# Optimization experiments

Hardware: AMD Instinct MI355X
Metric: run time of the kernel (lower is better)

## Reference

```python
import jax, jax.numpy as jnp
import numpy as np

B, S, D, H, MRP = 2, 2048, 1024, 16, 128
DK = D // H
NUM_REL = 2 * MRP + 1


def setup_inputs() -> dict:
    key = jax.random.key(0)
    ks = jax.random.split(key, 14)
    w = lambda k, shp: (jax.random.normal(k, shp, jnp.float32) * 0.02)
    return {
        'query': jax.random.normal(ks[0], (B, S, D), jnp.float32),
        'key':   jax.random.normal(ks[1], (B, S, D), jnp.float32),
        'value': jax.random.normal(ks[2], (B, S, D), jnp.float32),
        'Wq': w(ks[3], (D, D)), 'bq': jnp.zeros((D,), jnp.float32),
        'Wk': w(ks[4], (D, D)), 'bk': jnp.zeros((D,), jnp.float32),
        'Wv': w(ks[5], (D, D)), 'bv': jnp.zeros((D,), jnp.float32),
        'Wo': w(ks[6], (D, D)), 'bo': jnp.zeros((D,), jnp.float32),
        'rel_k': w(ks[7], (NUM_REL, DK)),
        'rel_v': w(ks[8], (NUM_REL, DK)),
    }


def reference(query, key, value, Wq, bq, Wk, bk, Wv, bv, Wo, bo, rel_k, rel_v):
    b, s, d = query.shape
    h, dk = H, DK
    # projections -> (b, h, s, dk)
    Q = (query @ Wq.T + bq).reshape(b, s, h, dk).transpose(0, 2, 1, 3)
    K = (key   @ Wk.T + bk).reshape(b, s, h, dk).transpose(0, 2, 1, 3)
    V = (value @ Wv.T + bv).reshape(b, s, h, dk).transpose(0, 2, 1, 3)
    # relative position indices: distance(i,j) = j - i, clipped, shifted to [0, 2*MRP]
    pos = jnp.arange(s)
    rel_idx = jnp.clip(pos[None, :] - pos[:, None], -MRP, MRP) + MRP  # (s, s)
    rk = rel_k[rel_idx]  # (s, s, dk)
    rv = rel_v[rel_idx]  # (s, s, dk)
    # content scores + relative-key scores
    scores = jnp.einsum('bhqd,bhkd->bhqk', Q, K)
    scores = scores + jnp.einsum('bhqd,qkd->bhqk', Q, rk)
    scores = scores * (1.0 / np.sqrt(dk).astype(np.float32))
    attn = jax.nn.softmax(scores, axis=-1)  # (b, h, s, s)
    # content context + relative-value context
    ctx = jnp.einsum('bhqk,bhkd->bhqd', attn, V)
    ctx = ctx + jnp.einsum('bhqk,qkd->bhqd', attn, rv)
    ctx = ctx.transpose(0, 2, 1, 3).reshape(b, s, d)
    out = ctx @ Wo.T + bo
    return out, attn
```

## Files before the change

kernel.cpp:

```cpp
#include <hip/hip_runtime.h>
#include <hip/hip_bf16.h>
#include <cstdint>
#include <cstddef>

using u16 = unsigned short;
using u32 = unsigned int;

typedef float f32x4 __attribute__((ext_vector_type(4)));
typedef short s16x8 __attribute__((ext_vector_type(8)));
typedef _Float16 f16x8 __attribute__((ext_vector_type(8)));
typedef unsigned short u16x4 __attribute__((ext_vector_type(4)));
typedef u32 u32x4 __attribute__((ext_vector_type(4)));

constexpr int Bc  = 2;
constexpr int Sc  = 2048;
constexpr int Dc  = 1024;
constexpr int Hc  = 16;
constexpr int DKc = 64;
constexpr int BHc = Bc * Hc;
constexpr int NREL = 257;
constexpr int RKROWS = 272;
constexpr int RVCOLS = 288;

constexpr float QSCALE = 0.125f * 1.4426950408889634f;

__device__ __forceinline__ u16 f2bf(float x){
  return __builtin_bit_cast(u16, __float2bfloat16(x));
}
__device__ __forceinline__ float bf2f(u16 u){
  return __builtin_bit_cast(float, (u32)u << 16);
}
__device__ __forceinline__ u16 f2h(float x){
  return __builtin_bit_cast(u16, (_Float16)x);
}
__device__ __forceinline__ u32 packh2(float a, float b){
  u16 x = __builtin_bit_cast(u16, (_Float16)a);
  u16 y = __builtin_bit_cast(u16, (_Float16)b);
  return (u32)x | ((u32)y << 16);
}
__device__ __forceinline__ float h2f_lo(u32 w){
  return (float)__builtin_bit_cast(_Float16, (u16)(w & 0xffffu));
}
__device__ __forceinline__ float h2f_hi(u32 w){
  return (float)__builtin_bit_cast(_Float16, (u16)(w >> 16));
}
__device__ __forceinline__ f32x4 mfma16(s16x8 a, s16x8 b, f32x4 c){
  return __builtin_amdgcn_mfma_f32_16x16x32_bf16(a, b, c, 0, 0, 0);
}
__device__ __forceinline__ f32x4 mfma16h(f16x8 a, f16x8 b, f32x4 c){
  return __builtin_amdgcn_mfma_f32_16x16x32_f16(a, b, c, 0, 0, 0);
}
__device__ __forceinline__ s16x8 ld8(const u16* p){
  return *reinterpret_cast<const s16x8*>(p);
}
__device__ __forceinline__ f16x8 ld8h(const u16* p){
  return *reinterpret_cast<const f16x8*>(p);
}
__device__ __forceinline__ void st_bf8(u16* p, float4 a, float4 b){
  s16x8 t;
  t[0] = (short)f2bf(a.x); t[1] = (short)f2bf(a.y);
  t[2] = (short)f2bf(a.z); t[3] = (short)f2bf(a.w);
  t[4] = (short)f2bf(b.x); t[5] = (short)f2bf(b.y);
  t[6] = (short)f2bf(b.z); t[7] = (short)f2bf(b.w);
  *reinterpret_cast<s16x8*>(p) = t;
}

__global__ void prep_rel(const float* __restrict__ rel_k,
                         const float* __restrict__ rel_v,
                         u16* __restrict__ relkb, u16* __restrict__ relvT)
{
  int tid = blockIdx.x * blockDim.x + threadIdx.x;
  int nthr = gridDim.x * blockDim.x;
  for (int i = tid; i < RKROWS * DKc; i += nthr){
    int r = i >> 6, c = i & 63;
    float v = (r < NREL) ? rel_k[r * DKc + c] : 0.0f;
    relkb[i] = f2bf(v);
  }
  for (int i = tid; i < DKc * RVCOLS; i += nthr){
    int d = i / RVCOLS, j = i - d * RVCOLS;
    float v = (j < NREL) ? rel_v[j * DKc + d] : 0.0f;
    relvT[i] = f2h(v);
  }
}

__global__ __launch_bounds__(256, 4) void proj_gemm(
    const float* __restrict__ Xq, const float* __restrict__ Xk, const float* __restrict__ Xv,
    const float* __restrict__ Wq, const float* __restrict__ Wk, const float* __restrict__ Wv,
    const float* __restrict__ bq, const float* __restrict__ bk, const float* __restrict__ bv,
    u16* __restrict__ Qb, u16* __restrict__ Kb, u16* __restrict__ Vt)
{
  const int type = blockIdx.y;
  const float* X    = (type == 0) ? Xq : (type == 1) ? Xk : Xv;
  const float* W    = (type == 0) ? Wq : (type == 1) ? Wk : Wv;
  const float* bias = (type == 0) ? bq : (type == 1) ? bk : bv;

  const int m0 = (int)(blockIdx.x >> 4) * 64;
  const int n0 = (int)(blockIdx.x & 15) * 64;

  __shared__ alignas(16) u16 As[64][56];
  __shared__ alignas(16) u16 Bs[64][56];

  const int tid  = threadIdx.x;
  const int wid  = tid >> 6, lane = tid & 63;
  const int lgrp = lane >> 4, lidx = lane & 15;
  const int wr   = wid >> 1,  wc   = wid & 1;

  const int srow = tid >> 2;
  const int scol = (tid & 3) << 3;

  f32x4 acc[2][2] = {};

  for (int it = 0; it < Dc / 32; ++it){
    const int k0 = it * 32;
    const float* xa = &X[(size_t)(m0 + srow) * Dc + k0 + scol];
    const float* xb = &W[(size_t)(n0 + srow) * Dc + k0 + scol];
    float4 a0 = *reinterpret_cast<const float4*>(xa);
    float4 a1 = *reinterpret_cast<const float4*>(xa + 4);
    float4 b0 = *reinterpret_cast<const float4*>(xb);
    float4 b1 = *reinterpret_cast<const float4*>(xb + 4);
    __syncthreads();
    st_bf8(&As[srow][scol], a0, a1);
    st_bf8(&Bs[srow][scol], b0, b1);
    __syncthreads();
    s16x8 af0 = ld8(&As[wr * 32 + lidx][lgrp * 8]);
    s16x8 af1 = ld8(&As[wr * 32 + 16 + lidx][lgrp * 8]);
    s16x8 bf0 = ld8(&Bs[wc * 32 + lidx][lgrp * 8]);
    s16x8 bf1 = ld8(&Bs[wc * 32 + 16 + lidx][lgrp * 8]);
    acc[0][0] = mfma16(af0, bf0, acc[0][0]);
    acc[0][1] = mfma16(af0, bf1, acc[0][1]);
    acc[1][0] = mfma16(af1, bf0, acc[1][0]);
    acc[1][1] = mfma16(af1, bf1, acc[1][1]);
  }

#pragma unroll
  for (int fm = 0; fm < 2; ++fm)
#pragma unroll
    for (int fn = 0; fn < 2; ++fn)
#pragma unroll
      for (int r = 0; r < 4; ++r){
        int mRow = m0 + wr * 32 + fm * 16 + lgrp * 4 + r;
        int nCol = n0 + wc * 32 + fn * 16 + lidx;
        float v = acc[fm][fn][r] + bias[nCol];
        int b = mRow >> 11, s = mRow & (Sc - 1);
        int h = nCol >> 6,  dk = nCol & 63;
        int bh = b * Hc + h;
        if (type == 0)      Qb[((size_t)bh * Sc + s) * DKc + dk] = f2bf(v * QSCALE);
        else if (type == 1) Kb[((size_t)bh * Sc + s) * DKc + dk] = f2bf(v);
        else                Vt[((size_t)bh * DKc + dk) * Sc + s] = f2h(v);
      }
}

__global__ __launch_bounds__(512, 4) void attn_fused(
    const u16* __restrict__ Qb, const u16* __restrict__ Kb, const u16* __restrict__ Vt,
    const u16* __restrict__ relkb, const u16* __restrict__ relvT,
    float* __restrict__ attn_out, u16* __restrict__ ctxb)
{
  __shared__ alignas(16) char smem[23232];
  u16 (*Rld)[260]   = reinterpret_cast<u16(*)[260]>(smem);
  u16 (*Ag)[288]    = reinterpret_cast<u16(*)[288]>(smem + 8320);
  float* red        = reinterpret_cast<float*>(smem + 17536);
  float* rscRow     = reinterpret_cast<float*>(smem + 19072);
  float (*ctxS)[64] = reinterpret_cast<float(*)[64]>(smem + 19136);
  u32*  Pw          = reinterpret_cast<u32*>(smem);

  const int tid  = threadIdx.x;
  const int wid  = tid >> 6, lane = tid & 63;
  const int lgrp = lane >> 4, lidx = lane & 15;

  const int flat    = (int)blockIdx.x;
  const int logical = (flat & 7) * 512 + (flat >> 3);
  const int bh      = logical >> 7;
  const int qtile   = logical & 127;
  const int q0      = qtile * 16;
  const int kbase   = wid * 256;

  const u16* Qp = Qb + (size_t)bh * Sc * DKc;
  const u16* Kp = Kb + (size_t)bh * Sc * DKc;
  const u16* Vp = Vt + (size_t)bh * DKc * Sc;
  float* attp   = attn_out + (size_t)bh * Sc * Sc;

  s16x8 aq0 = ld8(&Qp[(size_t)(q0 + lidx) * DKc + lgrp * 8]);
  s16x8 aq1 = ld8(&Qp[(size_t)(q0 + lidx) * DKc + 32 + lgrp * 8]);

  for (int jt = wid; jt < 17; jt += 8){
    int j0 = jt * 16;
    s16x8 b0 = ld8(&relkb[(size_t)(j0 + lidx) * DKc + lgrp * 8]);
    s16x8 b1 = ld8(&relkb[(size_t)(j0 + lidx) * DKc + 32 + lgrp * 8]);
    f32x4 rr = {0.f, 0.f, 0.f, 0.f};
    rr = mfma16(aq0, b0, rr);
    rr = mfma16(aq1, b1, rr);
    int j = j0 + lidx;
    if (j <= 256){
#pragma unroll
      for (int t = 0; t < 4; ++t) Rld[lgrp * 4 + t][j] = f2bf(rr[t]);
    }
  }
  {
    u32* agp = reinterpret_cast<u32*>(&Ag[0][0]);
    for (int i = tid; i < 16 * 288 / 2; i += 512) agp[i] = 0u;
  }
  __syncthreads();

  const float RloL = bf2f(Rld[lidx][0]);
  const float RhiL = bf2f(Rld[lidx][256]);
  const int kperm = ((lidx >> 2) << 3) + (lidx & 3);

  u32x4 pw[8];
  f32x4 cacc[4] = {};
  float l = 0.f, clow = 0.f, chigh = 0.f;

#pragma unroll
  for (int kb = 0; kb < 8; ++kb){
    const int kO = kbase + kb * 32;
    const bool all_lo = (kO + 31 - q0) <= -128;
    const bool all_hi = (kO - (q0 + 15)) >= 128;
    const u16* kr = &Kp[(size_t)(kO + kperm) * DKc];
    s16x8 bk00 = ld8(kr + lgrp * 8);
    s16x8 bk01 = ld8(kr + 32 + lgrp * 8);
    s16x8 bk10 = ld8(kr + 4 * DKc + lgrp * 8);
    s16x8 bk11 = ld8(kr + 4 * DKc + 32 + lgrp * 8);
    f16x8 bv0 = ld8h(&Vp[(size_t)(lidx) * Sc + kO + lgrp * 8]);
    f16x8 bv1 = ld8h(&Vp[(size_t)(16 + lidx) * Sc + kO + lgrp * 8]);
    f16x8 bv2 = ld8h(&Vp[(size_t)(32 + lidx) * Sc + kO + lgrp * 8]);
    f16x8 bv3 = ld8h(&Vp[(size_t)(48 + lidx) * Sc + kO + lgrp * 8]);

    f32x4 a0 = {0.f, 0.f, 0.f, 0.f}, a1 = {0.f, 0.f, 0.f, 0.f};
    a0 = mfma16(bk00, aq0, a0); a0 = mfma16(bk01, aq1, a0);
    a1 = mfma16(bk10, aq0, a1); a1 = mfma16(bk11, aq1, a1);

    float pu[8];
    if (all_lo | all_hi){
      const float addv = all_lo ? RloL : RhiL;
#pragma unroll
      for (int j = 0; j < 4; ++j){
        pu[j]     = __builtin_amdgcn_exp2f(a0[j] + addv);
        pu[j + 4] = __builtin_amdgcn_exp2f(a1[j] + addv);
      }
      float ps = ((pu[0] + pu[1]) + (pu[2] + pu[3])) + ((pu[4] + pu[5]) + (pu[6] + pu[7]));
      if (all_lo) clow += ps; else chigh += ps;
      l += ps;
    } else {
      const int dd0 = kO + lgrp * 8 - (q0 + lidx);
#pragma unroll
      for (int j = 0; j < 8; ++j){
        int dd = dd0 + j;
        float add = (dd <= -128) ? RloL : (dd >= 128) ? RhiL : bf2f(Rld[lidx][dd + 128]);
        float av = (j < 4) ? a0[j] : a1[j - 4];
        float p = __builtin_amdgcn_exp2f(av + add);
        pu[j] = p;
        if (dd <= -128)      clow  += p;
        else if (dd >= 128)  chigh += p;
        else                 Ag[lidx][dd + 128] = f2h(p);
      }
      l += ((pu[0] + pu[1]) + (pu[2] + pu[3])) + ((pu[4] + pu[5]) + (pu[6] + pu[7]));
    }
    u32x4 w4 = {packh2(pu[0], pu[1]), packh2(pu[2], pu[3]),
                packh2(pu[4], pu[5]), packh2(pu[6], pu[7])};
    pw[kb] = w4;
    f16x8 ap = __builtin_bit_cast(f16x8, w4);
    cacc[0] = mfma16h(ap, bv0, cacc[0]);
    cacc[1] = mfma16h(ap, bv1, cacc[1]);
    cacc[2] = mfma16h(ap, bv2, cacc[2]);
    cacc[3] = mfma16h(ap, bv3, cacc[3]);
  }

  l     += __shfl_xor(l, 16);      l     += __shfl_xor(l, 32);
  clow  += __shfl_xor(clow, 16);   clow  += __shfl_xor(clow, 32);
  chigh += __shfl_xor(chigh, 16);  chigh += __shfl_xor(chigh, 32);
  if (lane < 16){
    red[wid * 16 + lidx]       = l;
    red[128 + wid * 16 + lidx] = clow;
    red[256 + wid * 16 + lidx] = chigh;
  }
  __syncthreads();
  if (tid < 16){
    float s = 0.f, cl = 0.f, ch = 0.f;
#pragma unroll
    for (int w = 0; w < 8; ++w){
      s  += red[w * 16 + tid];
      cl += red[128 + w * 16 + tid];
      ch += red[256 + w * 16 + tid];
    }
    rscRow[tid] = 1.0f / s;
    Ag[tid][0]   = f2h(cl);
    Ag[tid][256] = f2h(ch);
  }
  __syncthreads();

  for (int t = wid; t < 9; t += 8){
    const int j0 = t * 32;
    f16x8 aa = ld8h(&Ag[lidx][j0 + lgrp * 8]);
#pragma unroll
    for (int dg = 0; dg < 4; ++dg){
      f16x8 bb = ld8h(&relvT[(size_t)(dg * 16 + lidx) * RVCOLS + j0 + lgrp * 8]);
      cacc[dg] = mfma16h(aa, bb, cacc[dg]);
    }
  }
#pragma unroll
  for (int dg = 0; dg < 4; ++dg)
#pragma unroll
    for (int r = 0; r < 4; ++r) cacc[dg][r] *= rscRow[lgrp * 4 + r];

  __syncthreads();

  {
    u32* PwW = Pw + wid * 512;
    const int xsw = (lidx & 7) << 2;
#pragma unroll
    for (int qt = 0; qt < 4; ++qt){
#pragma unroll
      for (int b = 0; b < 2; ++b){
        int csw = (b * 16 + lgrp * 4) ^ xsw;
        *reinterpret_cast<u32x4*>(&PwW[lidx * 32 + csw]) = pw[qt * 2 + b];
      }
      __asm__ volatile("" ::: "memory");
#pragma unroll
      for (int i = 0; i < 4; ++i){
        const int row = (lane >> 3) + 8 * (i >> 1);
        const int c0  = (((lane & 7) * 2 + (i & 1) * 16)) ^ ((row & 7) << 2);
        u32 w0 = PwW[row * 32 + c0];
        u32 w1 = PwW[row * 32 + c0 + 1];
        float sc_ = rscRow[row];
        f32x4 o;
        o[0] = h2f_lo(w0) * sc_;
        o[1] = h2f_hi(w0) * sc_;
        o[2] = h2f_lo(w1) * sc_;
        o[3] = h2f_hi(w1) * sc_;
        __builtin_nontemporal_store(o, reinterpret_cast<f32x4*>(
            &attp[(size_t)(q0 + row) * Sc + kbase + qt * 64 + (i & 1) * 32 + (lane & 7) * 4]));
      }
      __asm__ volatile("" ::: "memory");
    }
  }

  for (int w = 0; w < 8; ++w){
    if (wid == w){
#pragma unroll
      for (int dg = 0; dg < 4; ++dg)
#pragma unroll
        for (int r = 0; r < 4; ++r){
          const int row = lgrp * 4 + r, col = dg * 16 + lidx;
          if (w == 0) ctxS[row][col] = cacc[dg][r];
          else        ctxS[row][col] += cacc[dg][r];
        }
    }
    __syncthreads();
  }

  if (tid < 256){
    const int row2 = tid >> 4, qd = tid & 15;
    f32x4 sum = *reinterpret_cast<f32x4*>(&ctxS[row2][qd * 4]);
    const int b = bh >> 4, h = bh & 15;
    u16x4 o;
#pragma unroll
    for (int i = 0; i < 4; ++i) o[i] = f2bf(sum[i]);
    *reinterpret_cast<u16x4*>(&ctxb[((size_t)(b * Sc + q0 + row2)) * Dc + h * 64 + qd * 4]) = o;
  }
}

__global__ __launch_bounds__(256, 4) void out_gemm(
    const u16* __restrict__ A, const float* __restrict__ W,
    const float* __restrict__ bias, float* __restrict__ out)
{
  const int m0 = (int)(blockIdx.x >> 4) * 64;
  const int n0 = (int)(blockIdx.x & 15) * 64;

  __shared__ alignas(16) u16 As[64][56];
  __shared__ alignas(16) u16 Bs[64][56];

  const int tid  = threadIdx.x;
  const int wid  = tid >> 6, lane = tid & 63;
  const int lgrp = lane >> 4, lidx = lane & 15;
  const int wr   = wid >> 1,  wc   = wid & 1;
  const int srow = tid >> 2;
  const int scol = (tid & 3) << 3;

  f32x4 acc[2][2] = {};

  for (int it = 0; it < Dc / 32; ++it){
    const int k0 = it * 32;
    s16x8 av = ld8(&A[(size_t)(m0 + srow) * Dc + k0 + scol]);
    const float* xb = &W[(size_t)(n0 + srow) * Dc + k0 + scol];
    float4 b0 = *reinterpret_cast<const float4*>(xb);
    float4 b1 = *reinterpret_cast<const float4*>(xb + 4);
    __syncthreads();
    *reinterpret_cast<s16x8*>(&As[srow][scol]) = av;
    st_bf8(&Bs[srow][scol], b0, b1);
    __syncthreads();
    s16x8 af0 = ld8(&As[wr * 32 + lidx][lgrp * 8]);
    s16x8 af1 = ld8(&As[wr * 32 + 16 + lidx][lgrp * 8]);
    s16x8 bf0 = ld8(&Bs[wc * 32 + lidx][lgrp * 8]);
    s16x8 bf1 = ld8(&Bs[wc * 32 + 16 + lidx][lgrp * 8]);
    acc[0][0] = mfma16(af0, bf0, acc[0][0]);
    acc[0][1] = mfma16(af0, bf1, acc[0][1]);
    acc[1][0] = mfma16(af1, bf0, acc[1][0]);
    acc[1][1] = mfma16(af1, bf1, acc[1][1]);
  }

#pragma unroll
  for (int fm = 0; fm < 2; ++fm)
#pragma unroll
    for (int fn = 0; fn < 2; ++fn)
#pragma unroll
      for (int r = 0; r < 4; ++r){
        int mRow = m0 + wr * 32 + fm * 16 + lgrp * 4 + r;
        int nCol = n0 + wc * 32 + fn * 16 + lidx;
        out[(size_t)mRow * Dc + nCol] = acc[fm][fn][r] + bias[nCol];
      }
}

extern "C" void kernel_launch(void* const* d_in, const int* in_sizes, int n_in,
                              void* d_out, int out_size, void* d_ws, size_t ws_size,
                              hipStream_t stream)
{
  const float* query = (const float*)d_in[0];
  const float* key_  = (const float*)d_in[1];
  const float* value = (const float*)d_in[2];
  const float* Wq    = (const float*)d_in[3];
  const float* bq    = (const float*)d_in[4];
  const float* Wk    = (const float*)d_in[5];
  const float* bk    = (const float*)d_in[6];
  const float* Wv    = (const float*)d_in[7];
  const float* bv    = (const float*)d_in[8];
  const float* Wo    = (const float*)d_in[9];
  const float* bo    = (const float*)d_in[10];
  const float* rel_k = (const float*)d_in[11];
  const float* rel_v = (const float*)d_in[12];

  float* outp  = (float*)d_out;
  float* attnp = outp + (size_t)Bc * Sc * Dc;

  u16* Qb    = (u16*)d_ws;
  u16* Kb    = Qb + (size_t)BHc * Sc * DKc;
  u16* Vt    = Kb + (size_t)BHc * Sc * DKc;
  u16* ctxb  = Vt + (size_t)BHc * Sc * DKc;
  u16* relkb = ctxb + (size_t)Bc * Sc * Dc;
  u16* relvT = relkb + (size_t)RKROWS * DKc;

  prep_rel<<<dim3(32), dim3(256), 0, stream>>>(rel_k, rel_v, relkb, relvT);
  proj_gemm<<<dim3((Bc * Sc / 64) * (Dc / 64), 3), dim3(256), 0, stream>>>(
      query, key_, value, Wq, Wk, Wv, bq, bk, bv, Qb, Kb, Vt);
  attn_fused<<<dim3((Sc / 16) * BHc), dim3(512), 0, stream>>>(
      Qb, Kb, Vt, relkb, relvT, attnp, ctxb);
  out_gemm<<<dim3((Bc * Sc / 64) * (Dc / 64)), dim3(256), 0, stream>>>(
      ctxb, Wo, bo, outp);
}
```

Measured before the change: 392.9 us.

## Process two query tiles per block and overlap attn streamout with next tile compute

Each attention block now handles two 16-row query tiles in sequence. The probability write-out of the first tile is deferred into the second iteration, so its global stores can overlap the second tile's QK/softmax/PV work. The Pw staging buffer gets its own LDS region to make that possible, and __syncthreads is replaced by a custom lgkmcnt-wait plus s_barrier macro. The cost is more LDS per block (which may lower occupancy), half as many blocks in the grid, and reliance on the hand-written barrier being correct for global-memory ordering.

```diff
diff --git a/kernel.cpp b/kernel.cpp
--- a/kernel.cpp
+++ b/kernel.cpp
@@ -23,6 +23,8 @@
 constexpr int RVCOLS = 288;
 
 constexpr float QSCALE = 0.125f * 1.4426950408889634f;
+
+#define LGKM_BARRIER() __asm__ volatile("s_waitcnt lgkmcnt(0)\ns_barrier" ::: "memory")
 
 __device__ __forceinline__ u16 f2bf(float x){
   return __builtin_bit_cast(u16, __float2bfloat16(x));
@@ -155,23 +157,22 @@
     const u16* __restrict__ relkb, const u16* __restrict__ relvT,
     float* __restrict__ attn_out, u16* __restrict__ ctxb)
 {
-  __shared__ alignas(16) char smem[23232];
+  __shared__ alignas(16) char smem[39616];
   u16 (*Rld)[260]   = reinterpret_cast<u16(*)[260]>(smem);
   u16 (*Ag)[288]    = reinterpret_cast<u16(*)[288]>(smem + 8320);
   float* red        = reinterpret_cast<float*>(smem + 17536);
   float* rscRow     = reinterpret_cast<float*>(smem + 19072);
   float (*ctxS)[64] = reinterpret_cast<float(*)[64]>(smem + 19136);
-  u32*  Pw          = reinterpret_cast<u32*>(smem);
+  u32*  Pw          = reinterpret_cast<u32*>(smem + 23232);
 
   const int tid  = threadIdx.x;
   const int wid  = tid >> 6, lane = tid & 63;
   const int lgrp = lane >> 4, lidx = lane & 15;
 
   const int flat    = (int)blockIdx.x;
-  const int logical = (flat & 7) * 512 + (flat >> 3);
-  const int bh      = logical >> 7;
-  const int qtile   = logical & 127;
-  const int q0      = qtile * 16;
+  const int logical = (flat & 7) * 256 + (flat >> 3);
+  const int bh      = logical >> 6;
+  const int q0base  = (logical & 63) * 32;
   const int kbase   = wid * 256;
 
   const u16* Qp = Qb + (size_t)bh * Sc * DKc;
@@ -179,131 +180,12 @@
   const u16* Vp = Vt + (size_t)bh * DKc * Sc;
   float* attp   = attn_out + (size_t)bh * Sc * Sc;
 
-  s16x8 aq0 = ld8(&Qp[(size_t)(q0 + lidx) * DKc + lgrp * 8]);
-  s16x8 aq1 = ld8(&Qp[(size_t)(q0 + lidx) * DKc + 32 + lgrp * 8]);
-
-  for (int jt = wid; jt < 17; jt += 8){
-    int j0 = jt * 16;
-    s16x8 b0 = ld8(&relkb[(size_t)(j0 + lidx) * DKc + lgrp * 8]);
-    s16x8 b1 = ld8(&relkb[(size_t)(j0 + lidx) * DKc + 32 + lgrp * 8]);
-    f32x4 rr = {0.f, 0.f, 0.f, 0.f};
-    rr = mfma16(aq0, b0, rr);
-    rr = mfma16(aq1, b1, rr);
-    int j = j0 + lidx;
-    if (j <= 256){
-#pragma unroll
-      for (int t = 0; t < 4; ++t) Rld[lgrp * 4 + t][j] = f2bf(rr[t]);
-    }
-  }
-  {
-    u32* agp = reinterpret_cast<u32*>(&Ag[0][0]);
-    for (int i = tid; i < 16 * 288 / 2; i += 512) agp[i] = 0u;
-  }
-  __syncthreads();
-
-  const float RloL = bf2f(Rld[lidx][0]);
-  const float RhiL = bf2f(Rld[lidx][256]);
   const int kperm = ((lidx >> 2) << 3) + (lidx & 3);
+  const int b_out = bh >> 4, h_out = bh & 15;
 
   u32x4 pw[8];
-  f32x4 cacc[4] = {};
-  float l = 0.f, clow = 0.f, chigh = 0.f;
-
-#pragma unroll
-  for (int kb = 0; kb < 8; ++kb){
-    const int kO = kbase + kb * 32;
-    const bool all_lo = (kO + 31 - q0) <= -128;
-    const bool all_hi = (kO - (q0 + 15)) >= 128;
-    const u16* kr = &Kp[(size_t)(kO + kperm) * DKc];
-    s16x8 bk00 = ld8(kr + lgrp * 8);
-    s16x8 bk01 = ld8(kr + 32 + lgrp * 8);
-    s16x8 bk10 = ld8(kr + 4 * DKc + lgrp * 8);
-    s16x8 bk11 = ld8(kr + 4 * DKc + 32 + lgrp * 8);
-    f16x8 bv0 = ld8h(&Vp[(size_t)(lidx) * Sc + kO + lgrp * 8]);
-    f16x8 bv1 = ld8h(&Vp[(size_t)(16 + lidx) * Sc + kO + lgrp * 8]);
-    f16x8 bv2 = ld8h(&Vp[(size_t)(32 + lidx) * Sc + kO + lgrp * 8]);
-    f16x8 bv3 = ld8h(&Vp[(size_t)(48 + lidx) * Sc + kO + lgrp * 8]);
-
-    f32x4 a0 = {0.f, 0.f, 0.f, 0.f}, a1 = {0.f, 0.f, 0.f, 0.f};
-    a0 = mfma16(bk00, aq0, a0); a0 = mfma16(bk01, aq1, a0);
-    a1 = mfma16(bk10, aq0, a1); a1 = mfma16(bk11, aq1, a1);
-
-    float pu[8];
-    if (all_lo | all_hi){
-      const float addv = all_lo ? RloL : RhiL;
-#pragma unroll
-      for (int j = 0; j < 4; ++j){
-        pu[j]     = __builtin_amdgcn_exp2f(a0[j] + addv);
-        pu[j + 4] = __builtin_amdgcn_exp2f(a1[j] + addv);
-      }
-      float ps = ((pu[0] + pu[1]) + (pu[2] + pu[3])) + ((pu[4] + pu[5]) + (pu[6] + pu[7]));
-      if (all_lo) clow += ps; else chigh += ps;
-      l += ps;
-    } else {
-      const int dd0 = kO + lgrp * 8 - (q0 + lidx);
-#pragma unroll
-      for (int j = 0; j < 8; ++j){
-        int dd = dd0 + j;
-        float add = (dd <= -128) ? RloL : (dd >= 128) ? RhiL : bf2f(Rld[lidx][dd + 128]);
-        float av = (j < 4) ? a0[j] : a1[j - 4];
-        float p = __builtin_amdgcn_exp2f(av + add);
-        pu[j] = p;
-        if (dd <= -128)      clow  += p;
-        else if (dd >= 128)  chigh += p;
-        else                 Ag[lidx][dd + 128] = f2h(p);
-      }
-      l += ((pu[0] + pu[1]) + (pu[2] + pu[3])) + ((pu[4] + pu[5]) + (pu[6] + pu[7]));
-    }
-    u32x4 w4 = {packh2(pu[0], pu[1]), packh2(pu[2], pu[3]),
-                packh2(pu[4], pu[5]), packh2(pu[6], pu[7])};
-    pw[kb] = w4;
-    f16x8 ap = __builtin_bit_cast(f16x8, w4);
-    cacc[0] = mfma16h(ap, bv0, cacc[0]);
-    cacc[1] = mfma16h(ap, bv1, cacc[1]);
-    cacc[2] = mfma16h(ap, bv2, cacc[2]);
-    cacc[3] = mfma16h(ap, bv3, cacc[3]);
-  }
-
-  l     += __shfl_xor(l, 16);      l     += __shfl_xor(l, 32);
-  clow  += __shfl_xor(clow, 16);   clow  += __shfl_xor(clow, 32);
-  chigh += __shfl_xor(chigh, 16);  chigh += __shfl_xor(chigh, 32);
-  if (lane < 16){
-    red[wid * 16 + lidx]       = l;
-    red[128 + wid * 16 + lidx] = clow;
-    red[256 + wid * 16 + lidx] = chigh;
-  }
-  __syncthreads();
-  if (tid < 16){
-    float s = 0.f, cl = 0.f, ch = 0.f;
-#pragma unroll
-    for (int w = 0; w < 8; ++w){
-      s  += red[w * 16 + tid];
-      cl += red[128 + w * 16 + tid];
-      ch += red[256 + w * 16 + tid];
-    }
-    rscRow[tid] = 1.0f / s;
-    Ag[tid][0]   = f2h(cl);
-    Ag[tid][256] = f2h(ch);
-  }
-  __syncthreads();
-
-  for (int t = wid; t < 9; t += 8){
-    const int j0 = t * 32;
-    f16x8 aa = ld8h(&Ag[lidx][j0 + lgrp * 8]);
-#pragma unroll
-    for (int dg = 0; dg < 4; ++dg){
-      f16x8 bb = ld8h(&relvT[(size_t)(dg * 16 + lidx) * RVCOLS + j0 + lgrp * 8]);
-      cacc[dg] = mfma16h(aa, bb, cacc[dg]);
-    }
-  }
-#pragma unroll
-  for (int dg = 0; dg < 4; ++dg)
-#pragma unroll
-    for (int r = 0; r < 4; ++r) cacc[dg][r] *= rscRow[lgrp * 4 + r];
-
-  __syncthreads();
-
-  {
+
+  auto streamout = [&](int q0u){
     u32* PwW = Pw + wid * 512;
     const int xsw = (lidx & 7) << 2;
 #pragma unroll
@@ -327,35 +209,163 @@
         o[2] = h2f_lo(w1) * sc_;
         o[3] = h2f_hi(w1) * sc_;
         __builtin_nontemporal_store(o, reinterpret_cast<f32x4*>(
-            &attp[(size_t)(q0 + row) * Sc + kbase + qt * 64 + (i & 1) * 32 + (lane & 7) * 4]));
+            &attp[(size_t)(q0u + row) * Sc + kbase + qt * 64 + (i & 1) * 32 + (lane & 7) * 4]));
       }
       __asm__ volatile("" ::: "memory");
     }
+  };
+
+#pragma unroll 1
+  for (int unit = 0; unit < 2; ++unit){
+    const int q0 = q0base + unit * 16;
+
+    if (unit == 1) streamout(q0base);
+
+    s16x8 aq0 = ld8(&Qp[(size_t)(q0 + lidx) * DKc + lgrp * 8]);
+    s16x8 aq1 = ld8(&Qp[(size_t)(q0 + lidx) * DKc + 32 + lgrp * 8]);
+
+    for (int jt = wid; jt < 17; jt += 8){
+      int j0 = jt * 16;
+      s16x8 b0 = ld8(&relkb[(size_t)(j0 + lidx) * DKc + lgrp * 8]);
+      s16x8 b1 = ld8(&relkb[(size_t)(j0 + lidx) * DKc + 32 + lgrp * 8]);
+      f32x4 rr = {0.f, 0.f, 0.f, 0.f};
+      rr = mfma16(aq0, b0, rr);
+      rr = mfma16(aq1, b1, rr);
+      int j = j0 + lidx;
+      if (j <= 256){
+#pragma unroll
+        for (int t = 0; t < 4; ++t) Rld[lgrp * 4 + t][j] = f2bf(rr[t]);
+      }
+    }
+    {
+      u32* agp = reinterpret_cast<u32*>(&Ag[0][0]);
+      for (int i = tid; i < 16 * 288 / 2; i += 512) agp[i] = 0u;
+    }
+    LGKM_BARRIER();
+
+    const float RloL = bf2f(Rld[lidx][0]);
+    const float RhiL = bf2f(Rld[lidx][256]);
+
+    f32x4 cacc[4] = {};
+    float l = 0.f, clow = 0.f, chigh = 0.f;
+
+#pragma unroll
+    for (int kb = 0; kb < 8; ++kb){
+      const int kO = kbase + kb * 32;
+      const bool all_lo = (kO + 31 - q0) <= -128;
+      const bool all_hi = (kO - (q0 + 15)) >= 128;
+      const u16* kr = &Kp[(size_t)(kO + kperm) * DKc];
+      s16x8 bk00 = ld8(kr + lgrp * 8);
+      s16x8 bk01 = ld8(kr + 32 + lgrp * 8);
+      s16x8 bk10 = ld8(kr + 4 * DKc + lgrp * 8);
+      s16x8 bk11 = ld8(kr + 4 * DKc + 32 + lgrp * 8);
+      f16x8 bv0 = ld8h(&Vp[(size_t)(lidx) * Sc + kO + lgrp * 8]);
+      f16x8 bv1 = ld8h(&Vp[(size_t)(16 + lidx) * Sc + kO + lgrp * 8]);
+      f16x8 bv2 = ld8h(&Vp[(size_t)(32 + lidx) * Sc + kO + lgrp * 8]);
+      f16x8 bv3 = ld8h(&Vp[(size_t)(48 + lidx) * Sc + kO + lgrp * 8]);
+
+      f32x4 a0 = {0.f, 0.f, 0.f, 0.f}, a1 = {0.f, 0.f, 0.f, 0.f};
+      a0 = mfma16(bk00, aq0, a0); a0 = mfma16(bk01, aq1, a0);
+      a1 = mfma16(bk10, aq0, a1); a1 = mfma16(bk11, aq1, a1);
+
+      float pu[8];
+      if (all_lo | all_hi){
+        const float addv = all_lo ? RloL : RhiL;
+#pragma unroll
+        for (int j = 0; j < 4; ++j){
+          pu[j]     = __builtin_amdgcn_exp2f(a0[j] + addv);
+          pu[j + 4] = __builtin_amdgcn_exp2f(a1[j] + addv);
+        }
+        float ps = ((pu[0] + pu[1]) + (pu[2] + pu[3])) + ((pu[4] + pu[5]) + (pu[6] + pu[7]));
+        if (all_lo) clow += ps; else chigh += ps;
+        l += ps;
+      } else {
+        const int dd0 = kO + lgrp * 8 - (q0 + lidx);
+#pragma unroll
+        for (int j = 0; j < 8; ++j){
+          int dd = dd0 + j;
+          float add = (dd <= -128) ? RloL : (dd >= 128) ? RhiL : bf2f(Rld[lidx][dd + 128]);
+          float av = (j < 4) ? a0[j] : a1[j - 4];
+          float p = __builtin_amdgcn_exp2f(av + add);
+          pu[j] = p;
+          if (dd <= -128)      clow  += p;
+          else if (dd >= 128)  chigh += p;
+          else                 Ag[lidx][dd + 128] = f2h(p);
+        }
+        l += ((pu[0] + pu[1]) + (pu[2] + pu[3])) + ((pu[4] + pu[5]) + (pu[6] + pu[7]));
+      }
+      u32x4 w4 = {packh2(pu[0], pu[1]), packh2(pu[2], pu[3]),
+                  packh2(pu[4], pu[5]), packh2(pu[6], pu[7])};
+      pw[kb] = w4;
+      f16x8 ap = __builtin_bit_cast(f16x8, w4);
+      cacc[0] = mfma16h(ap, bv0, cacc[0]);
+      cacc[1] = mfma16h(ap, bv1, cacc[1]);
+      cacc[2] = mfma16h(ap, bv2, cacc[2]);
+      cacc[3] = mfma16h(ap, bv3, cacc[3]);
+    }
+
+    l     += __shfl_xor(l, 16);      l     += __shfl_xor(l, 32);
+    clow  += __shfl_xor(clow, 16);   clow  += __shfl_xor(clow, 32);
+    chigh += __shfl_xor(chigh, 16);  chigh += __shfl_xor(chigh, 32);
+    if (lane < 16){
+      red[wid * 16 + lidx]       = l;
+      red[128 + wid * 16 + lidx] = clow;
+      red[256 + wid * 16 + lidx] = chigh;
+    }
+    LGKM_BARRIER();
+    if (tid < 16){
+      float s = 0.f, cl = 0.f, ch = 0.f;
+#pragma unroll
+      for (int w = 0; w < 8; ++w){
+        s  += red[w * 16 + tid];
+        cl += red[128 + w * 16 + tid];
+        ch += red[256 + w * 16 + tid];
+      }
+      rscRow[tid] = 1.0f / s;
+      Ag[tid][0]   = f2h(cl);
+      Ag[tid][256] = f2h(ch);
+    }
+    LGKM_BARRIER();
+
+    for (int t = wid; t < 9; t += 8){
+      const int j0 = t * 32;
+      f16x8 aa = ld8h(&Ag[lidx][j0 + lgrp * 8]);
+#pragma unroll
+      for (int dg = 0; dg < 4; ++dg){
+        f16x8 bb = ld8h(&relvT[(size_t)(dg * 16 + lidx) * RVCOLS + j0 + lgrp * 8]);
+        cacc[dg] = mfma16h(aa, bb, cacc[dg]);
+      }
+    }
+#pragma unroll
+    for (int dg = 0; dg < 4; ++dg)
+#pragma unroll
+      for (int r = 0; r < 4; ++r) cacc[dg][r] *= rscRow[lgrp * 4 + r];
+
+    for (int w = 0; w < 8; ++w){
+      if (wid == w){
+#pragma unroll
+        for (int dg = 0; dg < 4; ++dg)
+#pragma unroll
+          for (int r = 0; r < 4; ++r){
+            const int row = lgrp * 4 + r, col = dg * 16 + lidx;
+            if (w == 0) ctxS[row][col] = cacc[dg][r];
+            else        ctxS[row][col] += cacc[dg][r];
+          }
+      }
+      LGKM_BARRIER();
+    }
+    if (tid < 256){
+      const int row2 = tid >> 4, qd = tid & 15;
+      f32x4 sum = *reinterpret_cast<f32x4*>(&ctxS[row2][qd * 4]);
+      u16x4 o;
+#pragma unroll
+      for (int i = 0; i < 4; ++i) o[i] = f2bf(sum[i]);
+      *reinterpret_cast<u16x4*>(
+          &ctxb[((size_t)(b_out * Sc + q0 + row2)) * Dc + h_out * 64 + qd * 4]) = o;
+    }
   }
 
-  for (int w = 0; w < 8; ++w){
-    if (wid == w){
-#pragma unroll
-      for (int dg = 0; dg < 4; ++dg)
-#pragma unroll
-        for (int r = 0; r < 4; ++r){
-          const int row = lgrp * 4 + r, col = dg * 16 + lidx;
-          if (w == 0) ctxS[row][col] = cacc[dg][r];
-          else        ctxS[row][col] += cacc[dg][r];
-        }
-    }
-    __syncthreads();
-  }
-
-  if (tid < 256){
-    const int row2 = tid >> 4, qd = tid & 15;
-    f32x4 sum = *reinterpret_cast<f32x4*>(&ctxS[row2][qd * 4]);
-    const int b = bh >> 4, h = bh & 15;
-    u16x4 o;
-#pragma unroll
-    for (int i = 0; i < 4; ++i) o[i] = f2bf(sum[i]);
-    *reinterpret_cast<u16x4*>(&ctxb[((size_t)(b * Sc + q0 + row2)) * Dc + h * 64 + qd * 4]) = o;
-  }
+  streamout(q0base + 16);
 }
 
 __global__ __launch_bounds__(256, 4) void out_gemm(
@@ -440,7 +450,7 @@
   prep_rel<<<dim3(32), dim3(256), 0, stream>>>(rel_k, rel_v, relkb, relvT);
   proj_gemm<<<dim3((Bc * Sc / 64) * (Dc / 64), 3), dim3(256), 0, stream>>>(
       query, key_, value, Wq, Wk, Wv, bq, bk, bv, Qb, Kb, Vt);
-  attn_fused<<<dim3((Sc / 16) * BHc), dim3(512), 0, stream>>>(
+  attn_fused<<<dim3((Sc / 32) * BHc), dim3(512), 0, stream>>>(
       Qb, Kb, Vt, relkb, relvT, attnp, ctxb);
   out_gemm<<<dim3((Bc * Sc / 64) * (Dc / 64)), dim3(256), 0, stream>>>(
       ctxb, Wo, bo, outp);
```

Measured after the change: 598.3 us. +52.3%, slower.
